# Kernel optimization log

Hardware: AMD Instinct MI355X
Metric: run time of the kernel (lower is better)

Reference implementation:

```python
import jax, jax.numpy as jnp
import numpy as np

N = 50000      # nodes
E = 800000     # edges
F_IN = 128     # num_features
H = 64         # hidden_dim
G = 64         # graphs in batch
EPS = 1e-5


def setup_inputs() -> dict:
    ks = jax.random.split(jax.random.key(0), 16)
    x = jax.random.normal(ks[0], (N, F_IN), dtype=jnp.float32)
    edge_index = jax.random.randint(ks[1], (2, E), 0, N, dtype=jnp.int64)
    batch = jnp.sort(jax.random.randint(ks[2], (N,), 0, G, dtype=jnp.int64))
    s = 0.05
    inp = {"x": x, "edge_index": edge_index, "batch": batch}
    # GCNConv layers: W [out,in], bias [out]; BatchNorm gamma/beta [H]
    dims = [(H, F_IN), (H, H), (H, H)]
    for i, (o, ci) in enumerate(dims):
        inp[f"W{i}"] = jax.random.normal(ks[3 + i], (o, ci), dtype=jnp.float32) * s
        inp[f"b{i}"] = jnp.zeros((o,), dtype=jnp.float32)
        inp[f"g{i}"] = jnp.ones((o,), dtype=jnp.float32)
        inp[f"be{i}"] = jnp.zeros((o,), dtype=jnp.float32)
    inp["lin1_w"] = jax.random.normal(ks[10], (H // 2, H), dtype=jnp.float32) * s
    inp["lin1_b"] = jnp.zeros((H // 2,), dtype=jnp.float32)
    inp["lin2_w"] = jax.random.normal(ks[11], (1, H // 2), dtype=jnp.float32) * s
    inp["lin2_b"] = jnp.zeros((1,), dtype=jnp.float32)
    return inp


def _gcn_conv(x, src, dst, W, b):
    # PyG GCNConv: h = x W^T; add self-loops; symmetric deg^{-1/2} norm; scatter-add; + bias
    h = x @ W.T                                   # [N, out]
    n = x.shape[0]
    deg = jax.ops.segment_sum(jnp.ones(src.shape[0], h.dtype), dst, num_segments=n) + 1.0
    dinv = jax.lax.rsqrt(deg)                     # [N]
    msg = h[src] * (dinv[src] * dinv[dst])[:, None]   # per-edge messages
    agg = jax.ops.segment_sum(msg, dst, num_segments=n)
    agg = agg + h * (dinv * dinv)[:, None]        # self-loop contribution
    return agg + b


def _bn_relu(x, g, be):
    # BatchNorm1d (training-mode batch stats, biased var) + ReLU; dropout = identity (eval)
    m = x.mean(axis=0)
    v = jnp.var(x, axis=0)
    return jax.nn.relu((x - m) * jax.lax.rsqrt(v + EPS) * g + be)


def reference(x, edge_index, batch,
              W0, b0, g0, be0, W1, b1, g1, be1, W2, b2, g2, be2,
              lin1_w, lin1_b, lin2_w, lin2_b):
    src, dst = edge_index[0], edge_index[1]
    Ws = [(W0, b0, g0, be0), (W1, b1, g1, be1), (W2, b2, g2, be2)]
    h = x
    for (W, b, g, be) in Ws:
        h = _bn_relu(_gcn_conv(h, src, dst, W, b), g, be)
    # global mean pool over graphs
    sums = jax.ops.segment_sum(h, batch, num_segments=G)          # [G, H]
    cnt = jax.ops.segment_sum(jnp.ones((h.shape[0],), h.dtype), batch, num_segments=G)
    pooled = sums / jnp.maximum(cnt, 1.0)[:, None]
    h = jax.nn.relu(pooled @ lin1_w.T + lin1_b)
    return h @ lin2_w.T + lin2_b                                   # [G, 1]
```

## Files before the change

### kernel.cpp

```cpp
#include <hip/hip_runtime.h>

#define NN 50000
#define NE 800000
#define FIN 128
#define H 64
#define NG 64
#define BN_EPS 1e-5f
#define INV_N (1.0f / 50000.0f)
#define NBKT 196
#define PB 256
#define SLICE 64
#define BKCAP 8192
#define PROWS 16
#define NSEG 4

__device__ __forceinline__ void f4acc(float4& a, const float4 b) {
    a.x += b.x; a.y += b.y; a.z += b.z; a.w += b.w;
}
__device__ __forceinline__ void f4accw(float4& a, const float4 b, float w) {
    a.x += b.x * w; a.y += b.y * w; a.z += b.z * w; a.w += b.w * w;
}

__global__ void prep(const float* __restrict__ W0, const float* __restrict__ W1,
                     const float* __restrict__ W2, const int* __restrict__ src,
                     const int* __restrict__ dst, float* __restrict__ Wt0,
                     float* __restrict__ Wt1, float* __restrict__ Wt2,
                     float* __restrict__ sl0, float* __restrict__ sl1,
                     float* __restrict__ sl2, float* __restrict__ pool,
                     float* __restrict__ cnt, int* __restrict__ cnts,
                     unsigned int* __restrict__ staged) {
    const int tid = threadIdx.x, bid = blockIdx.x;
    const int gtid = bid * 256 + tid;
    const int gsz = PB * 256;
    for (int i = gtid; i < 64 * 128; i += gsz) { sl0[i] = 0.f; sl1[i] = 0.f; sl2[i] = 0.f; }
    for (int i = gtid; i < NG * H; i += gsz) pool[i] = 0.f;
    if (gtid < NG) cnt[gtid] = 0.f;
    for (int i = gtid; i < FIN * 64; i += gsz) {
        int k = i >> 6, o = i & 63;
        Wt0[i] = W0[o * FIN + k];
    }
    for (int i = gtid; i < H * 64; i += gsz) {
        int k = i >> 6, o = i & 63;
        Wt1[i] = W1[o * H + k];
        Wt2[i] = W2[o * H + k];
    }
    __shared__ int hcnt[NBKT];
    for (int i = tid; i < NBKT; i += 256) hcnt[i] = 0;
    __syncthreads();
    const int chunk = NE / PB;
    const int e0 = bid * chunk, e1 = e0 + chunk;
    for (int e = e0 + tid; e < e1; e += 256) {
        int d = dst[e];
        int s = src[e];
        int bkt = d >> 8;
        int idx = atomicAdd(&hcnt[bkt], 1);
        if (idx < SLICE)
            staged[(size_t)(bkt * PB + bid) * SLICE + idx] =
                (unsigned int)s | ((unsigned int)(d & 255) << 16);
    }
    __syncthreads();
    for (int i = tid; i < NBKT; i += 256) cnts[i * PB + bid] = min(hcnt[i], SLICE);
}

union CsrMmSh {
    struct { float Xs[64 * 68]; float Ws[64 * 64]; } mm;
    struct { int cnt[256]; int loc[256]; int cur[256]; int spre[257]; } csr;
};

__device__ __forceinline__ int slice_find(const int* __restrict__ spre, int t) {
    int lo = 0, hi = 255;
    while (lo < hi) {
        int mid = (lo + hi + 1) >> 1;
        if (spre[mid] <= t) lo = mid; else hi = mid - 1;
    }
    return lo;
}

template <int K, bool SEGIN>
__device__ __forceinline__ void mm_tile_body(int base, const float* __restrict__ x,
                                             const float* __restrict__ Wtg,
                                             const float* __restrict__ slots,
                                             const float* __restrict__ gamma,
                                             const float* __restrict__ beta,
                                             const float* __restrict__ dv,
                                             float* __restrict__ outp, float* Xs, float* Ws,
                                             float* st, int n) {
    const int tid = threadIdx.x;
    if (slots) {
        if (tid < 128) {
            float s0 = 0.f, s1 = 0.f, s2 = 0.f, s3 = 0.f;
            for (int k = 0; k < 64; k += 4) {
                s0 += slots[(k + 0) * 128 + tid];
                s1 += slots[(k + 1) * 128 + tid];
                s2 += slots[(k + 2) * 128 + tid];
                s3 += slots[(k + 3) * 128 + tid];
            }
            st[tid] = (s0 + s1) + (s2 + s3);
        }
        __syncthreads();
    }
    const int q = tid >> 4;
    const int co = (tid & 15) * 4;
    const int kq = (tid & 15) * 4;
    float4 a0 = make_float4(0.f, 0.f, 0.f, 0.f);
    float4 a1 = a0, a2 = a0, a3 = a0;

    for (int kc = 0; kc < K; kc += 64) {
        if (kc) __syncthreads();
        for (int i = tid; i < 64 * 64; i += 256) Ws[i] = Wtg[kc * 64 + i];
        {
            const int kidx = kc + kq;
            float4 sc = make_float4(1.f, 1.f, 1.f, 1.f);
            float4 sh = make_float4(0.f, 0.f, 0.f, 0.f);
            if (slots) {
                float4 s = *(const float4*)&st[kidx];
                float4 ss = *(const float4*)&st[64 + kidx];
                float4 gm = *(const float4*)&gamma[kidx];
                float4 bt = *(const float4*)&beta[kidx];
                float mx = s.x * INV_N, my = s.y * INV_N, mz = s.z * INV_N, mw = s.w * INV_N;
                sc.x = gm.x * rsqrtf(ss.x * INV_N - mx * mx + BN_EPS);
                sc.y = gm.y * rsqrtf(ss.y * INV_N - my * my + BN_EPS);
                sc.z = gm.z * rsqrtf(ss.z * INV_N - mz * mz + BN_EPS);
                sc.w = gm.w * rsqrtf(ss.w * INV_N - mw * mw + BN_EPS);
                sh.x = bt.x - mx * sc.x;
                sh.y = bt.y - my * sc.y;
                sh.z = bt.z - mz * sc.z;
                sh.w = bt.w - mw * sc.w;
            }
            for (int j = 0; j < 4; ++j) {
                int r = (tid >> 4) + j * 16;
                int row = base + r;
                float4 v = make_float4(0.f, 0.f, 0.f, 0.f);
                if (row < n) {
                    if (SEGIN)
                        v = *(const float4*)&x[((size_t)(kidx >> 4) * NN + row) * 16 + (kidx & 15)];
                    else
                        v = *(const float4*)&x[(size_t)row * K + kidx];
                }
                if (slots) {
                    v.x = fmaxf(v.x * sc.x + sh.x, 0.f);
                    v.y = fmaxf(v.y * sc.y + sh.y, 0.f);
                    v.z = fmaxf(v.z * sc.z + sh.z, 0.f);
                    v.w = fmaxf(v.w * sc.w + sh.w, 0.f);
                }
                *(float4*)&Xs[r * 68 + kq] = v;
            }
        }
        __syncthreads();

#pragma unroll 2
        for (int k = 0; k < 64; k += 4) {
            float4 x0 = *(const float4*)&Xs[(q + 0) * 68 + k];
            float4 x1 = *(const float4*)&Xs[(q + 16) * 68 + k];
            float4 x2 = *(const float4*)&Xs[(q + 32) * 68 + k];
            float4 x3 = *(const float4*)&Xs[(q + 48) * 68 + k];
            float4 w0 = *(const float4*)&Ws[(k + 0) * 64 + co];
            float4 w1 = *(const float4*)&Ws[(k + 1) * 64 + co];
            float4 w2 = *(const float4*)&Ws[(k + 2) * 64 + co];
            float4 w3 = *(const float4*)&Ws[(k + 3) * 64 + co];

            a0.x += x0.x * w0.x + x0.y * w1.x + x0.z * w2.x + x0.w * w3.x;
            a0.y += x0.x * w0.y + x0.y * w1.y + x0.z * w2.y + x0.w * w3.y;
            a0.z += x0.x * w0.z + x0.y * w1.z + x0.z * w2.z + x0.w * w3.z;
            a0.w += x0.x * w0.w + x0.y * w1.w + x0.z * w2.w + x0.w * w3.w;

            a1.x += x1.x * w0.x + x1.y * w1.x + x1.z * w2.x + x1.w * w3.x;
            a1.y += x1.x * w0.y + x1.y * w1.y + x1.z * w2.y + x1.w * w3.y;
            a1.z += x1.x * w0.z + x1.y * w1.z + x1.z * w2.z + x1.w * w3.z;
            a1.w += x1.x * w0.w + x1.y * w1.w + x1.z * w2.w + x1.w * w3.w;

            a2.x += x2.x * w0.x + x2.y * w1.x + x2.z * w2.x + x2.w * w3.x;
            a2.y += x2.x * w0.y + x2.y * w1.y + x2.z * w2.y + x2.w * w3.y;
            a2.z += x2.x * w0.z + x2.y * w1.z + x2.z * w2.z + x2.w * w3.z;
            a2.w += x2.x * w0.w + x2.y * w1.w + x2.z * w2.w + x2.w * w3.w;

            a3.x += x3.x * w0.x + x3.y * w1.x + x3.z * w2.x + x3.w * w3.x;
            a3.y += x3.x * w0.y + x3.y * w1.y + x3.z * w2.y + x3.w * w3.y;
            a3.z += x3.x * w0.z + x3.y * w1.z + x3.z * w2.z + x3.w * w3.z;
            a3.w += x3.x * w0.w + x3.y * w1.w + x3.z * w2.w + x3.w * w3.w;
        }
    }

    const int sg = co >> 4, so = co & 15;
    int r0 = base + q;
    if (r0 < n) {
        float d = dv ? dv[r0] : 1.f;
        a0.x *= d; a0.y *= d; a0.z *= d; a0.w *= d;
        *(float4*)&outp[((size_t)sg * NN + r0) * 16 + so] = a0;
    }
    if (r0 + 16 < n) {
        float d = dv ? dv[r0 + 16] : 1.f;
        a1.x *= d; a1.y *= d; a1.z *= d; a1.w *= d;
        *(float4*)&outp[((size_t)sg * NN + r0 + 16) * 16 + so] = a1;
    }
    if (r0 + 32 < n) {
        float d = dv ? dv[r0 + 32] : 1.f;
        a2.x *= d; a2.y *= d; a2.z *= d; a2.w *= d;
        *(float4*)&outp[((size_t)sg * NN + r0 + 32) * 16 + so] = a2;
    }
    if (r0 + 48 < n) {
        float d = dv ? dv[r0 + 48] : 1.f;
        a3.x *= d; a3.y *= d; a3.z *= d; a3.w *= d;
        *(float4*)&outp[((size_t)sg * NN + r0 + 48) * 16 + so] = a3;
    }
}

__global__ __launch_bounds__(256, 4) void csr_mm0(
    const unsigned int* __restrict__ staged, const int* __restrict__ cnts,
    int* __restrict__ rs, int* __restrict__ re, float* __restrict__ dinv,
    int* __restrict__ csr, const float* __restrict__ x, const float* __restrict__ Wt0,
    float* __restrict__ bufA) {
    __shared__ CsrMmSh sh;
    const int tid = threadIdx.x;
    if (blockIdx.x < NBKT) {
        const int b = blockIdx.x;
        int c = cnts[b * PB + tid];
        sh.csr.loc[tid] = c;
        sh.csr.cnt[tid] = 0;
        __syncthreads();
        for (int off = 1; off < 256; off <<= 1) {
            int t = (tid >= off) ? sh.csr.loc[tid - off] : 0;
            __syncthreads();
            sh.csr.loc[tid] += t;
            __syncthreads();
        }
        sh.csr.spre[tid] = sh.csr.loc[tid] - c;
        if (tid == 255) sh.csr.spre[256] = sh.csr.loc[255];
        __syncthreads();
        const int T = sh.csr.spre[256];
        for (int t = tid; t < T; t += 256) {
            int s = slice_find(sh.csr.spre, t);
            unsigned int u = staged[(size_t)(b * PB + s) * SLICE + (t - sh.csr.spre[s])];
            atomicAdd(&sh.csr.cnt[(u >> 16) & 255], 1);
        }
        __syncthreads();
        int v = sh.csr.cnt[tid];
        sh.csr.loc[tid] = v;
        __syncthreads();
        for (int off = 1; off < 256; off <<= 1) {
            int t = (tid >= off) ? sh.csr.loc[tid - off] : 0;
            __syncthreads();
            sh.csr.loc[tid] += t;
            __syncthreads();
        }
        const int start = b * BKCAP + sh.csr.loc[tid] - v;
        const int node = b * 256 + tid;
        if (node < NN) {
            rs[node] = start;
            re[node] = start + v;
            dinv[node] = rsqrtf((float)v + 1.0f);
        }
        sh.csr.cur[tid] = start;
        __syncthreads();
        for (int t = tid; t < T; t += 256) {
            int s = slice_find(sh.csr.spre, t);
            unsigned int u = staged[(size_t)(b * PB + s) * SLICE + (t - sh.csr.spre[s])];
            int j = atomicAdd(&sh.csr.cur[(u >> 16) & 255], 1);
            csr[j] = (int)(u & 0xFFFFu);
        }
    } else {
        mm_tile_body<FIN, false>((blockIdx.x - NBKT) * 64, x, Wt0, nullptr, nullptr, nullptr,
                                 nullptr, bufA, sh.mm.Xs, sh.mm.Ws, nullptr, NN);
    }
}

__global__ __launch_bounds__(256, 4) void matmul_bn(const float* __restrict__ x,
                                                    const float* __restrict__ Wtg,
                                                    const float* __restrict__ slots,
                                                    const float* __restrict__ gamma,
                                                    const float* __restrict__ beta,
                                                    const float* __restrict__ dv,
                                                    float* __restrict__ outp, int n) {
    __shared__ float Xs[64 * 68];
    __shared__ float Ws[64 * 64];
    __shared__ __align__(16) float st[128];
    mm_tile_body<H, true>(blockIdx.x * 64, x, Wtg, slots, gamma, beta, dv, outp, Xs, Ws, st, n);
}

template <bool ED>
__global__ __launch_bounds__(256) void gather_seg(const float* __restrict__ h,
                                                  const int* __restrict__ rs,
                                                  const int* __restrict__ re,
                                                  const int* __restrict__ csrc,
                                                  const float* __restrict__ dv,
                                                  const float* __restrict__ bias,
                                                  float* __restrict__ outp,
                                                  float* __restrict__ slots, int seg) {
    const int tid = threadIdx.x;
    const int wv = tid >> 6;
    const int lane = tid & 63;
    const int fl = lane & 3;
    const int ss = (lane >> 2) & 3;
    const int ds = lane >> 4;
    const int d = (blockIdx.x * 4 + wv) * 4 + ds;
    const float* hseg = h + (size_t)seg * NN * 16;
    const int fo = fl * 4;
    const int j1 = re[d];
    const float dA = dv[d];
    float4 acc = make_float4(0.f, 0.f, 0.f, 0.f);
    int j = rs[d] + ss;
    while (j + 4 < j1) {
        int s0 = csrc[j], s1 = csrc[j + 4];
        if (ED) {
            f4accw(acc, *(const float4*)&hseg[(size_t)s0 * 16 + fo], dv[s0]);
            f4accw(acc, *(const float4*)&hseg[(size_t)s1 * 16 + fo], dv[s1]);
        } else {
            f4acc(acc, *(const float4*)&hseg[(size_t)s0 * 16 + fo]);
            f4acc(acc, *(const float4*)&hseg[(size_t)s1 * 16 + fo]);
        }
        j += 8;
    }
    if (j < j1) {
        int s0 = csrc[j];
        if (ED)
            f4accw(acc, *(const float4*)&hseg[(size_t)s0 * 16 + fo], dv[s0]);
        else
            f4acc(acc, *(const float4*)&hseg[(size_t)s0 * 16 + fo]);
    }
    acc.x += __shfl_xor(acc.x, 4); acc.x += __shfl_xor(acc.x, 8);
    acc.y += __shfl_xor(acc.y, 4); acc.y += __shfl_xor(acc.y, 8);
    acc.z += __shfl_xor(acc.z, 4); acc.z += __shfl_xor(acc.z, 8);
    acc.w += __shfl_xor(acc.w, 4); acc.w += __shfl_xor(acc.w, 8);
    const float4 self = *(const float4*)&hseg[(size_t)d * 16 + fo];
    const float4 bq = *(const float4*)&bias[seg * 16 + fo];
    const float sf = ED ? dA : 1.f;
    float4 v;
    v.x = bq.x + dA * (acc.x + sf * self.x);
    v.y = bq.y + dA * (acc.y + sf * self.y);
    v.z = bq.z + dA * (acc.z + sf * self.z);
    v.w = bq.w + dA * (acc.w + sf * self.w);
    if (ss == 0) *(float4*)&outp[((size_t)seg * NN + d) * 16 + fo] = v;
    __shared__ float4 red[2][4][4][4];
    if (ss == 0) {
        float4 vq;
        vq.x = v.x * v.x; vq.y = v.y * v.y; vq.z = v.z * v.z; vq.w = v.w * v.w;
        red[0][wv][ds][fl] = v;
        red[1][wv][ds][fl] = vq;
    }
    __syncthreads();
    if (tid < 8) {
        int a = tid >> 2, f2 = tid & 3;
        float4 s = make_float4(0.f, 0.f, 0.f, 0.f);
#pragma unroll
        for (int i = 0; i < 16; ++i) f4acc(s, red[a][i >> 2][i & 3][f2]);
        float* slot = slots + (blockIdx.x & 63) * 128 + a * 64 + seg * 16 + f2 * 4;
        atomicAdd(&slot[0], s.x);
        atomicAdd(&slot[1], s.y);
        atomicAdd(&slot[2], s.z);
        atomicAdd(&slot[3], s.w);
    }
}

__global__ void pool_seg(const float* __restrict__ h, const float* __restrict__ slots,
                         const float* __restrict__ gamma, const float* __restrict__ beta,
                         const int* __restrict__ batch, float* __restrict__ pool,
                         float* __restrict__ cnt, int n) {
    __shared__ __align__(16) float pst[128];
    if (threadIdx.x < 128) {
        float s0 = 0.f, s1 = 0.f, s2 = 0.f, s3 = 0.f;
        for (int k = 0; k < 64; k += 4) {
            s0 += slots[(k + 0) * 128 + threadIdx.x];
            s1 += slots[(k + 1) * 128 + threadIdx.x];
            s2 += slots[(k + 2) * 128 + threadIdx.x];
            s3 += slots[(k + 3) * 128 + threadIdx.x];
        }
        pst[threadIdx.x] = (s0 + s1) + (s2 + s3);
    }
    __syncthreads();
    int wave = blockIdx.x * 4 + (threadIdx.x >> 6);
    int c = threadIdx.x & 63;
    int r0 = wave * PROWS;
    if (r0 >= n) return;
    int r1 = min(r0 + PROWS, n);
    float mean = pst[c] * INV_N;
    float var = pst[64 + c] * INV_N - mean * mean;
    float sc = gamma[c] * rsqrtf(var + BN_EPS);
    float sh = beta[c] - mean * sc;
    const size_t segbase = (size_t)(c >> 4) * NN * 16 + (c & 15);
    int cur = batch[r0];
    float acc = 0.f;
    int nlocal = 0;
    for (int r = r0; r < r1; ++r) {
        int g = batch[r];
        if (g != cur) {
            atomicAdd(&pool[cur * H + c], acc);
            if (c == 0) atomicAdd(&cnt[cur], (float)nlocal);
            cur = g;
            acc = 0.f;
            nlocal = 0;
        }
        acc += fmaxf(h[segbase + (size_t)r * 16] * sc + sh, 0.f);
        ++nlocal;
    }
    atomicAdd(&pool[cur * H + c], acc);
    if (c == 0) atomicAdd(&cnt[cur], (float)nlocal);
}

__global__ void final_mlp(const float* __restrict__ pool, const float* __restrict__ cnt,
                          const float* __restrict__ l1w, const float* __restrict__ l1b,
                          const float* __restrict__ l2w, const float* __restrict__ l2b,
                          float* __restrict__ out) {
    int tid = blockIdx.x * 256 + threadIdx.x;
    int g = tid >> 5;
    int j = tid & 31;
    if (g >= NG) return;
    float inv = 1.0f / fmaxf(cnt[g], 1.0f);
    float s = l1b[j];
    for (int k = 0; k < H; ++k) s += pool[g * H + k] * inv * l1w[j * H + k];
    float v = fmaxf(s, 0.0f) * l2w[j];
    for (int off = 16; off > 0; off >>= 1) v += __shfl_down(v, off, 32);
    if (j == 0) out[g] = v + l2b[0];
}

extern "C" void kernel_launch(void* const* d_in, const int* in_sizes, int n_in,
                              void* d_out, int out_size, void* d_ws, size_t ws_size,
                              hipStream_t stream) {
    const float* x = (const float*)d_in[0];
    const int* ei = (const int*)d_in[1];
    const int* batch = (const int*)d_in[2];
    const float* W[3] = {(const float*)d_in[3], (const float*)d_in[7], (const float*)d_in[11]};
    const float* b[3] = {(const float*)d_in[4], (const float*)d_in[8], (const float*)d_in[12]};
    const float* g[3] = {(const float*)d_in[5], (const float*)d_in[9], (const float*)d_in[13]};
    const float* be[3] = {(const float*)d_in[6], (const float*)d_in[10], (const float*)d_in[14]};
    const float* l1w = (const float*)d_in[15];
    const float* l1b = (const float*)d_in[16];
    const float* l2w = (const float*)d_in[17];
    const float* l2b = (const float*)d_in[18];
    float* out = (float*)d_out;

    const int* src = ei;
    const int* dst = ei + NE;

    char* wsb = (char*)d_ws;
    size_t off = 0;
    auto alloc = [&](size_t elems) {
        void* p = wsb + off;
        off += elems * 4;
        return p;
    };
    float* dinv = (float*)alloc(50048);
    float* bufA = (float*)alloc((size_t)NN * H);
    float* bufB = (float*)alloc((size_t)NN * H);
    float* slots[3] = {(float*)alloc(64 * 128), (float*)alloc(64 * 128), (float*)alloc(64 * 128)};
    float* pool = (float*)alloc(NG * H);
    float* cnt = (float*)alloc(64);
    float* Wt[3] = {(float*)alloc(FIN * 64), (float*)alloc(H * 64), (float*)alloc(H * 64)};
    int* rs = (int*)alloc(50048);
    int* re = (int*)alloc(50048);
    int* cnts = (int*)alloc((size_t)NBKT * PB);
    unsigned int* staged = (unsigned int*)alloc((size_t)NBKT * PB * SLICE);
    int* csr = (int*)alloc((size_t)NBKT * BKCAP);

    const int grid_mm = (NN + 63) / 64;
    const int grid_gs = NN / 16;

    prep<<<PB, 256, 0, stream>>>(W[0], W[1], W[2], src, dst, Wt[0], Wt[1], Wt[2], slots[0],
                                 slots[1], slots[2], pool, cnt, cnts, staged);
    csr_mm0<<<NBKT + grid_mm, 256, 0, stream>>>(staged, cnts, rs, re, dinv, csr, x, Wt[0], bufA);
    for (int s = 0; s < NSEG; ++s)
        gather_seg<true><<<grid_gs, 256, 0, stream>>>(bufA, rs, re, csr, dinv, b[0], bufB,
                                                      slots[0], s);
    matmul_bn<<<grid_mm, 256, 0, stream>>>(bufB, Wt[1], slots[0], g[0], be[0], dinv, bufA, NN);
    for (int s = 0; s < NSEG; ++s)
        gather_seg<false><<<grid_gs, 256, 0, stream>>>(bufA, rs, re, csr, dinv, b[1], bufB,
                                                       slots[1], s);
    matmul_bn<<<grid_mm, 256, 0, stream>>>(bufB, Wt[2], slots[1], g[1], be[1], dinv, bufA, NN);
    for (int s = 0; s < NSEG; ++s)
        gather_seg<false><<<grid_gs, 256, 0, stream>>>(bufA, rs, re, csr, dinv, b[2], bufB,
                                                       slots[2], s);
    const int pool_grid = ((NN + PROWS - 1) / PROWS + 3) / 4;
    pool_seg<<<pool_grid, 256, 0, stream>>>(bufB, slots[2], g[2], be[2], batch, pool, cnt, NN);
    final_mlp<<<8, 256, 0, stream>>>(pool, cnt, l1w, l1b, l2w, l2b, out);
}
```

Baseline: 366.6 us.

## Use 8-column feature segments, 16-bit CSR indices, and single-launch segmented gather

Splits the hidden features into eight 8-wide column segments instead of four 16-wide ones, so each segment plane (50000 rows of 8 floats) fits better in cache during random neighbour gathers. CSR source indices are stored as 16-bit values, halving index traffic. The per-segment gather loop of launches becomes one kernel that picks the segment from the block id. It also uses two accumulators and a shuffle-based batch-norm statistics reduction to cut shared-memory work. The cost is that each edge's index and dinv are read twice as many times, once per segment, and the 8-float rows mean narrower 32-byte accesses per neighbour.

```diff
diff --git a/kernel.cpp b/kernel.cpp
--- a/kernel.cpp
+++ b/kernel.cpp
@@ -12,7 +12,7 @@
 #define SLICE 64
 #define BKCAP 8192
 #define PROWS 16
-#define NSEG 4
+#define NSEG 8
 
 __device__ __forceinline__ void f4acc(float4& a, const float4 b) {
     a.x += b.x; a.y += b.y; a.z += b.z; a.w += b.w;
@@ -133,7 +133,7 @@
                 float4 v = make_float4(0.f, 0.f, 0.f, 0.f);
                 if (row < n) {
                     if (SEGIN)
-                        v = *(const float4*)&x[((size_t)(kidx >> 4) * NN + row) * 16 + (kidx & 15)];
+                        v = *(const float4*)&x[((size_t)(kidx >> 3) * NN + row) * 8 + (kidx & 7)];
                     else
                         v = *(const float4*)&x[(size_t)row * K + kidx];
                 }
@@ -181,35 +181,35 @@
         }
     }
 
-    const int sg = co >> 4, so = co & 15;
+    const int sg = co >> 3, so = co & 7;
     int r0 = base + q;
     if (r0 < n) {
         float d = dv ? dv[r0] : 1.f;
         a0.x *= d; a0.y *= d; a0.z *= d; a0.w *= d;
-        *(float4*)&outp[((size_t)sg * NN + r0) * 16 + so] = a0;
+        *(float4*)&outp[((size_t)sg * NN + r0) * 8 + so] = a0;
     }
     if (r0 + 16 < n) {
         float d = dv ? dv[r0 + 16] : 1.f;
         a1.x *= d; a1.y *= d; a1.z *= d; a1.w *= d;
-        *(float4*)&outp[((size_t)sg * NN + r0 + 16) * 16 + so] = a1;
+        *(float4*)&outp[((size_t)sg * NN + r0 + 16) * 8 + so] = a1;
     }
     if (r0 + 32 < n) {
         float d = dv ? dv[r0 + 32] : 1.f;
         a2.x *= d; a2.y *= d; a2.z *= d; a2.w *= d;
-        *(float4*)&outp[((size_t)sg * NN + r0 + 32) * 16 + so] = a2;
+        *(float4*)&outp[((size_t)sg * NN + r0 + 32) * 8 + so] = a2;
     }
     if (r0 + 48 < n) {
         float d = dv ? dv[r0 + 48] : 1.f;
         a3.x *= d; a3.y *= d; a3.z *= d; a3.w *= d;
-        *(float4*)&outp[((size_t)sg * NN + r0 + 48) * 16 + so] = a3;
+        *(float4*)&outp[((size_t)sg * NN + r0 + 48) * 8 + so] = a3;
     }
 }
 
 __global__ __launch_bounds__(256, 4) void csr_mm0(
     const unsigned int* __restrict__ staged, const int* __restrict__ cnts,
     int* __restrict__ rs, int* __restrict__ re, float* __restrict__ dinv,
-    int* __restrict__ csr, const float* __restrict__ x, const float* __restrict__ Wt0,
-    float* __restrict__ bufA) {
+    unsigned short* __restrict__ csr, const float* __restrict__ x,
+    const float* __restrict__ Wt0, float* __restrict__ bufA) {
     __shared__ CsrMmSh sh;
     const int tid = threadIdx.x;
     if (blockIdx.x < NBKT) {
@@ -256,7 +256,7 @@
             int s = slice_find(sh.csr.spre, t);
             unsigned int u = staged[(size_t)(b * PB + s) * SLICE + (t - sh.csr.spre[s])];
             int j = atomicAdd(&sh.csr.cur[(u >> 16) & 255], 1);
-            csr[j] = (int)(u & 0xFFFFu);
+            csr[j] = (unsigned short)(u & 0xFFFFu);
         }
     } else {
         mm_tile_body<FIN, false>((blockIdx.x - NBKT) * 64, x, Wt0, nullptr, nullptr, nullptr,
@@ -278,72 +278,87 @@
 }
 
 template <bool ED>
-__global__ __launch_bounds__(256) void gather_seg(const float* __restrict__ h,
-                                                  const int* __restrict__ rs,
-                                                  const int* __restrict__ re,
-                                                  const int* __restrict__ csrc,
-                                                  const float* __restrict__ dv,
-                                                  const float* __restrict__ bias,
-                                                  float* __restrict__ outp,
-                                                  float* __restrict__ slots, int seg) {
+__global__ __launch_bounds__(256) void gather8(const float* __restrict__ h,
+                                               const int* __restrict__ rs,
+                                               const int* __restrict__ re,
+                                               const unsigned short* __restrict__ csrc,
+                                               const float* __restrict__ dv,
+                                               const float* __restrict__ bias,
+                                               float* __restrict__ outp,
+                                               float* __restrict__ slots) {
     const int tid = threadIdx.x;
+    const int bid = blockIdx.x;
+    const int seg = bid & 7;
     const int wv = tid >> 6;
     const int lane = tid & 63;
-    const int fl = lane & 3;
-    const int ss = (lane >> 2) & 3;
-    const int ds = lane >> 4;
-    const int d = (blockIdx.x * 4 + wv) * 4 + ds;
-    const float* hseg = h + (size_t)seg * NN * 16;
+    const int fl = lane & 1;
+    const int ss = (lane >> 1) & 3;
+    const int ds = lane >> 3;
+    const int d = (bid >> 3) * 32 + wv * 8 + ds;
+    const float* hseg = h + (size_t)seg * NN * 8;
     const int fo = fl * 4;
-    const int j1 = re[d];
-    const float dA = dv[d];
-    float4 acc = make_float4(0.f, 0.f, 0.f, 0.f);
-    int j = rs[d] + ss;
-    while (j + 4 < j1) {
-        int s0 = csrc[j], s1 = csrc[j + 4];
-        if (ED) {
-            f4accw(acc, *(const float4*)&hseg[(size_t)s0 * 16 + fo], dv[s0]);
-            f4accw(acc, *(const float4*)&hseg[(size_t)s1 * 16 + fo], dv[s1]);
-        } else {
-            f4acc(acc, *(const float4*)&hseg[(size_t)s0 * 16 + fo]);
-            f4acc(acc, *(const float4*)&hseg[(size_t)s1 * 16 + fo]);
-        }
-        j += 8;
-    }
-    if (j < j1) {
-        int s0 = csrc[j];
-        if (ED)
-            f4accw(acc, *(const float4*)&hseg[(size_t)s0 * 16 + fo], dv[s0]);
-        else
-            f4acc(acc, *(const float4*)&hseg[(size_t)s0 * 16 + fo]);
-    }
-    acc.x += __shfl_xor(acc.x, 4); acc.x += __shfl_xor(acc.x, 8);
-    acc.y += __shfl_xor(acc.y, 4); acc.y += __shfl_xor(acc.y, 8);
-    acc.z += __shfl_xor(acc.z, 4); acc.z += __shfl_xor(acc.z, 8);
-    acc.w += __shfl_xor(acc.w, 4); acc.w += __shfl_xor(acc.w, 8);
-    const float4 self = *(const float4*)&hseg[(size_t)d * 16 + fo];
-    const float4 bq = *(const float4*)&bias[seg * 16 + fo];
-    const float sf = ED ? dA : 1.f;
-    float4 v;
-    v.x = bq.x + dA * (acc.x + sf * self.x);
-    v.y = bq.y + dA * (acc.y + sf * self.y);
-    v.z = bq.z + dA * (acc.z + sf * self.z);
-    v.w = bq.w + dA * (acc.w + sf * self.w);
-    if (ss == 0) *(float4*)&outp[((size_t)seg * NN + d) * 16 + fo] = v;
-    __shared__ float4 red[2][4][4][4];
-    if (ss == 0) {
-        float4 vq;
-        vq.x = v.x * v.x; vq.y = v.y * v.y; vq.z = v.z * v.z; vq.w = v.w * v.w;
-        red[0][wv][ds][fl] = v;
-        red[1][wv][ds][fl] = vq;
+    float4 v = make_float4(0.f, 0.f, 0.f, 0.f);
+    if (d < NN) {
+        const int j1 = re[d];
+        const float dA = dv[d];
+        float4 acc = make_float4(0.f, 0.f, 0.f, 0.f);
+        float4 acc2 = acc;
+        int j = rs[d] + ss;
+        while (j + 4 < j1) {
+            int s0 = csrc[j], s1 = csrc[j + 4];
+            if (ED) {
+                f4accw(acc, *(const float4*)&hseg[(size_t)s0 * 8 + fo], dv[s0]);
+                f4accw(acc2, *(const float4*)&hseg[(size_t)s1 * 8 + fo], dv[s1]);
+            } else {
+                f4acc(acc, *(const float4*)&hseg[(size_t)s0 * 8 + fo]);
+                f4acc(acc2, *(const float4*)&hseg[(size_t)s1 * 8 + fo]);
+            }
+            j += 8;
+        }
+        if (j < j1) {
+            int s0 = csrc[j];
+            if (ED)
+                f4accw(acc, *(const float4*)&hseg[(size_t)s0 * 8 + fo], dv[s0]);
+            else
+                f4acc(acc, *(const float4*)&hseg[(size_t)s0 * 8 + fo]);
+        }
+        f4acc(acc, acc2);
+        acc.x += __shfl_xor(acc.x, 2); acc.x += __shfl_xor(acc.x, 4);
+        acc.y += __shfl_xor(acc.y, 2); acc.y += __shfl_xor(acc.y, 4);
+        acc.z += __shfl_xor(acc.z, 2); acc.z += __shfl_xor(acc.z, 4);
+        acc.w += __shfl_xor(acc.w, 2); acc.w += __shfl_xor(acc.w, 4);
+        const float4 self = *(const float4*)&hseg[(size_t)d * 8 + fo];
+        const float4 bq = *(const float4*)&bias[seg * 8 + fo];
+        const float sf = ED ? dA : 1.f;
+        v.x = bq.x + dA * (acc.x + sf * self.x);
+        v.y = bq.y + dA * (acc.y + sf * self.y);
+        v.z = bq.z + dA * (acc.z + sf * self.z);
+        v.w = bq.w + dA * (acc.w + sf * self.w);
+        if (ss == 0) *(float4*)&outp[((size_t)seg * NN + d) * 8 + fo] = v;
+    }
+    float4 q;
+    q.x = v.x * v.x; q.y = v.y * v.y; q.z = v.z * v.z; q.w = v.w * v.w;
+    v.x += __shfl_xor(v.x, 8); v.x += __shfl_xor(v.x, 16); v.x += __shfl_xor(v.x, 32);
+    v.y += __shfl_xor(v.y, 8); v.y += __shfl_xor(v.y, 16); v.y += __shfl_xor(v.y, 32);
+    v.z += __shfl_xor(v.z, 8); v.z += __shfl_xor(v.z, 16); v.z += __shfl_xor(v.z, 32);
+    v.w += __shfl_xor(v.w, 8); v.w += __shfl_xor(v.w, 16); v.w += __shfl_xor(v.w, 32);
+    q.x += __shfl_xor(q.x, 8); q.x += __shfl_xor(q.x, 16); q.x += __shfl_xor(q.x, 32);
+    q.y += __shfl_xor(q.y, 8); q.y += __shfl_xor(q.y, 16); q.y += __shfl_xor(q.y, 32);
+    q.z += __shfl_xor(q.z, 8); q.z += __shfl_xor(q.z, 16); q.z += __shfl_xor(q.z, 32);
+    q.w += __shfl_xor(q.w, 8); q.w += __shfl_xor(q.w, 16); q.w += __shfl_xor(q.w, 32);
+    __shared__ float4 red[2][4][2];
+    if (ss == 0 && ds == 0) {
+        red[0][wv][fl] = v;
+        red[1][wv][fl] = q;
     }
     __syncthreads();
-    if (tid < 8) {
-        int a = tid >> 2, f2 = tid & 3;
-        float4 s = make_float4(0.f, 0.f, 0.f, 0.f);
-#pragma unroll
-        for (int i = 0; i < 16; ++i) f4acc(s, red[a][i >> 2][i & 3][f2]);
-        float* slot = slots + (blockIdx.x & 63) * 128 + a * 64 + seg * 16 + f2 * 4;
+    if (tid < 4) {
+        int a = tid >> 1, f = tid & 1;
+        float4 s = red[a][0][f];
+        f4acc(s, red[a][1][f]);
+        f4acc(s, red[a][2][f]);
+        f4acc(s, red[a][3][f]);
+        float* slot = slots + ((bid >> 3) & 63) * 128 + a * 64 + seg * 8 + f * 4;
         atomicAdd(&slot[0], s.x);
         atomicAdd(&slot[1], s.y);
         atomicAdd(&slot[2], s.z);
@@ -376,7 +391,7 @@
     float var = pst[64 + c] * INV_N - mean * mean;
     float sc = gamma[c] * rsqrtf(var + BN_EPS);
     float sh = beta[c] - mean * sc;
-    const size_t segbase = (size_t)(c >> 4) * NN * 16 + (c & 15);
+    const size_t segbase = (size_t)(c >> 3) * NN * 8 + (c & 7);
     int cur = batch[r0];
     float acc = 0.f;
     int nlocal = 0;
@@ -389,7 +404,7 @@
             acc = 0.f;
             nlocal = 0;
         }
-        acc += fmaxf(h[segbase + (size_t)r * 16] * sc + sh, 0.f);
+        acc += fmaxf(h[segbase + (size_t)r * 8] * sc + sh, 0.f);
         ++nlocal;
     }
     atomicAdd(&pool[cur * H + c], acc);
@@ -449,25 +464,19 @@
     int* re = (int*)alloc(50048);
     int* cnts = (int*)alloc((size_t)NBKT * PB);
     unsigned int* staged = (unsigned int*)alloc((size_t)NBKT * PB * SLICE);
-    int* csr = (int*)alloc((size_t)NBKT * BKCAP);
+    unsigned short* csr = (unsigned short*)alloc((size_t)NBKT * BKCAP / 2);
 
     const int grid_mm = (NN + 63) / 64;
-    const int grid_gs = NN / 16;
+    const int grid_g8 = ((NN + 31) / 32) * NSEG;
 
     prep<<<PB, 256, 0, stream>>>(W[0], W[1], W[2], src, dst, Wt[0], Wt[1], Wt[2], slots[0],
                                  slots[1], slots[2], pool, cnt, cnts, staged);
     csr_mm0<<<NBKT + grid_mm, 256, 0, stream>>>(staged, cnts, rs, re, dinv, csr, x, Wt[0], bufA);
-    for (int s = 0; s < NSEG; ++s)
-        gather_seg<true><<<grid_gs, 256, 0, stream>>>(bufA, rs, re, csr, dinv, b[0], bufB,
-                                                      slots[0], s);
+    gather8<true><<<grid_g8, 256, 0, stream>>>(bufA, rs, re, csr, dinv, b[0], bufB, slots[0]);
     matmul_bn<<<grid_mm, 256, 0, stream>>>(bufB, Wt[1], slots[0], g[0], be[0], dinv, bufA, NN);
-    for (int s = 0; s < NSEG; ++s)
-        gather_seg<false><<<grid_gs, 256, 0, stream>>>(bufA, rs, re, csr, dinv, b[1], bufB,
-                                                       slots[1], s);
+    gather8<false><<<grid_g8, 256, 0, stream>>>(bufA, rs, re, csr, dinv, b[1], bufB, slots[1]);
     matmul_bn<<<grid_mm, 256, 0, stream>>>(bufB, Wt[2], slots[1], g[1], be[1], dinv, bufA, NN);
-    for (int s = 0; s < NSEG; ++s)
-        gather_seg<false><<<grid_gs, 256, 0, stream>>>(bufA, rs, re, csr, dinv, b[2], bufB,
-                                                       slots[2], s);
+    gather8<false><<<grid_g8, 256, 0, stream>>>(bufA, rs, re, csr, dinv, b[2], bufB, slots[2]);
     const int pool_grid = ((NN + PROWS - 1) / PROWS + 3) / 4;
     pool_seg<<<pool_grid, 256, 0, stream>>>(bufB, slots[2], g[2], be[2], batch, pool, cnt, NN);
     final_mlp<<<8, 256, 0, stream>>>(pool, cnt, l1w, l1b, l2w, l2b, out);
```

New measurement: 345.1 us. 5.9% less time.
